# Performance work log

Hardware: AMD Instinct MI355X
Metric: run time of the kernel (lower is better)

## Reference

```python
import jax, jax.numpy as jnp
import numpy as np

MARGIN = 0.0  # init kwarg margin=0


def setup_inputs() -> dict:
    key = jax.random.key(0)
    k1, k2 = jax.random.split(key)
    inputs = jax.random.normal(k1, (4096, 2048), dtype=jnp.float32)
    targets = jax.random.randint(k2, (4096,), 0, 64, dtype=jnp.int64)
    return {"inputs": inputs, "targets": targets}


def _last_true_index(cond):
    # cond: (n, n) bool. Original torch loop zeros leading True entries until one
    # remains -> keeps the LAST True index per row.
    n = cond.shape[1]
    return (n - 1) - jnp.argmax(cond[:, ::-1], axis=1)


def reference(inputs, targets):
    n = inputs.shape[0]
    INF = jnp.asarray(jnp.inf, dtype=inputs.dtype)

    # pairwise euclidean distances: ||xi||^2 + ||xj||^2 - 2 xi.xj, clamp, sqrt
    sq = jnp.sum(inputs * inputs, axis=1)
    dist = sq[:, None] + sq[None, :] - 2.0 * (inputs @ inputs.T)
    dist = jnp.sqrt(jnp.clip(dist, 1e-12))  # (n, n)

    same = targets[:, None] == targets[None, :]  # (n, n) same-label mask

    # hardest positive / hardest negative per row
    dist_ap = jnp.where(same, dist, -INF).max(axis=1)
    dist_an = jnp.where(same, INF, dist).min(axis=1)

    # tie-broken indices (last occurrence, matching the torch loop)
    p = _last_true_index((dist == dist_ap[:, None]) & same)      # hardest pos idx
    q = _last_true_index((dist == dist_an[:, None]) & (~same))   # hardest neg idx

    # an2 = dist(hardest_pos_i, hardest_neg_i)
    dist_an2 = dist[p, q]

    # maskc: labels differing from both anchor's label and hardest-negative's label
    lbl_q = targets[q]
    maskc = (targets[None, :] != targets[:, None]) & (targets[None, :] != lbl_q[:, None])

    dist_q = dist[q]  # (n, n): distance rows of the hardest negatives
    ok_min = jnp.where(maskc, dist_q, INF).min(axis=1)
    r = _last_true_index((dist_q == ok_min[:, None]) & maskc)

    dist_an3 = dist[jnp.arange(n), r]  # dist(anchor, third-class sample)
    dist_an4 = dist_q[jnp.arange(n), r]  # dist(hardest neg, third-class sample) == ok_min

    # MarginRankingLoss(margin, reduce=False) with y=1: relu(ap - an + margin)
    loss = jax.nn.relu(dist_ap - dist_an + MARGIN)
    loss3 = jnp.abs(dist_an - dist_an2)
    loss4 = jnp.abs(dist_an3 - dist_an4)
    return (loss + loss3 + loss4).sum() / n
```

## Files before the change

### kernel.cpp

```cpp
#include <hip/hip_runtime.h>
#include <hip/hip_bf16.h>
#include <cstdint>

#define N_DIM 4096
#define K_DIM 2048
#define NKT 32
#define QSCALE 24.0f
#define QINV (1.0f / 24.0f)

typedef float floatx4 __attribute__((ext_vector_type(4)));
typedef int intx4 __attribute__((ext_vector_type(4)));
typedef unsigned short ushort8 __attribute__((ext_vector_type(8)));
typedef unsigned long long ull;

__device__ __forceinline__ unsigned short f2bf(float f) {
    unsigned int u = __builtin_bit_cast(unsigned int, f);
    unsigned int r = (u + 0x7fffu + ((u >> 16) & 1u)) >> 16;
    return (unsigned short)r;
}

__device__ __forceinline__ float bf2f(unsigned short b) {
    return __uint_as_float(((unsigned)b) << 16);
}

__device__ __forceinline__ void gld_lds16(const void* g, void* l) {
    __builtin_amdgcn_global_load_lds(
        (const __attribute__((address_space(1))) unsigned int*)g,
        (__attribute__((address_space(3))) unsigned int*)l,
        16, 0, 0);
}

__global__ __launch_bounds__(256)
void prep_kernel(const float* __restrict__ X, char* __restrict__ Qt,
                 int* __restrict__ sqi) {
    const int row = blockIdx.x;
    const int tid = threadIdx.x;
    const float* xr = X + (size_t)row * K_DIM;
    floatx4 a = *(const floatx4*)(xr + tid * 8);
    floatx4 b = *(const floatx4*)(xr + tid * 8 + 4);
    int s = 0;
    unsigned lo = 0, hi = 0;
#pragma unroll
    for (int e = 0; e < 4; ++e) {
        int v = __float2int_rn(a[e] * QSCALE);
        v = min(127, max(-127, v));
        s += v * v;
        lo |= ((unsigned)(v & 0xff)) << (8 * e);
        int w = __float2int_rn(b[e] * QSCALE);
        w = min(127, max(-127, w));
        s += w * w;
        hi |= ((unsigned)(w & 0xff)) << (8 * e);
    }
    *(int2*)(Qt + ((size_t)(tid >> 1) * 4096 + row) * 16 + (tid & 1) * 8) =
        make_int2((int)lo, (int)hi);
#pragma unroll
    for (int off = 32; off; off >>= 1) s += __shfl_down(s, off);
    __shared__ int wsum[4];
    const int wave = tid >> 6, lane = tid & 63;
    if (lane == 0) wsum[wave] = s;
    __syncthreads();
    if (tid == 0) sqi[row] = wsum[0] + wsum[1] + wsum[2] + wsum[3];
}

#define BAR() __builtin_amdgcn_s_barrier()
#define PRIO1() __builtin_amdgcn_s_setprio(1)
#define PRIO0() __builtin_amdgcn_s_setprio(0)
#define VMCNT4() asm volatile("s_waitcnt vmcnt(4)" ::: "memory")
#define VMCNT0() asm volatile("s_waitcnt vmcnt(0)" ::: "memory")
#define MM8(MHI, AF) { _Pragma("unroll") for (int n_ = 0; n_ < 4; ++n_) { \
    _Pragma("unroll") for (int m_ = 0; m_ < 4; ++m_) { \
        acc[MHI][n_][m_] = __builtin_amdgcn_mfma_i32_16x16x64_i8( \
            AF[m_], bfv[n_], acc[MHI][n_][m_], 0, 0, 0); } } }
#define KTB 262144
#define STG_B(KT, BB) { \
    gld_lds16(bSt + (size_t)(KT) * KTB,        lds + (BB) + 16384 + widB); \
    gld_lds16(bSt + (size_t)(KT) * KTB + 2048, lds + (BB) + 24576 + widB); }
#define STG_A(KT, BB) { \
    gld_lds16(aSt + (size_t)(KT) * KTB,        lds + (BB) + widB); \
    gld_lds16(aSt + (size_t)(KT) * KTB + 2048, lds + (BB) + 8192 + widB); }

__global__ __launch_bounds__(512, 2)
void gemm_dist(const char* __restrict__ Qt, const int* __restrict__ sqi,
               unsigned short* __restrict__ Db) {
    __shared__ char lds[98304];
    const int tid = threadIdx.x;
    const int wid = tid >> 6, lane = tid & 63;
    const int wr = wid >> 2, wc = wid & 3;
    const int fr = lane & 15, ksub = lane >> 4;
    const int widB = wid * 1024;

    int rA[4], rB[4];
#pragma unroll
    for (int m = 0; m < 4; ++m) rA[m] = (ksub * 128 + m * 16 + fr) * 16;
#pragma unroll
    for (int n = 0; n < 4; ++n) rB[n] = (ksub * 128 + (wc & 1) * 64 + n * 16 + fr) * 16;
    const int aRegOff = wr * 8192;
    const int bRegOff = 16384 + (wc >> 1) * 8192;

    const int swz = (blockIdx.x & 7) * 32 + (blockIdx.x >> 3);
    const int bi = swz >> 4, bj = swz & 15;
    const int rowC0 = bi * 256, colC0 = bj * 256;

    const int srow = tid & 127;
    const int sks = tid >> 7;
    const char* aSt = Qt + ((size_t)sks * 4096 + rowC0 + srow) * 16;
    const char* bSt = Qt + ((size_t)sks * 4096 + colC0 + srow) * 16;

    intx4 acc[2][4][4];
#pragma unroll
    for (int a0 = 0; a0 < 2; ++a0)
#pragma unroll
    for (int a1 = 0; a1 < 4; ++a1)
#pragma unroll
    for (int a2 = 0; a2 < 4; ++a2) acc[a0][a1][a2] = (intx4){0, 0, 0, 0};
    intx4 aflo[4], afhi[4], bfv[4];

    STG_B(0, 0); STG_A(0, 0);
    STG_B(1, 32768); STG_A(1, 32768);
    VMCNT4();
    BAR();

    int cb = 0, sb = 65536;
    for (int t = 0; t < NKT; ++t) {
        const bool pf = (t < NKT - 2);
        const char* bufA = lds + cb + aRegOff;
        const char* bufBp = lds + cb + bRegOff;
#pragma unroll
        for (int m = 0; m < 4; ++m) aflo[m] = *(const intx4*)(bufA + rA[m]);
#pragma unroll
        for (int n = 0; n < 4; ++n) bfv[n] = *(const intx4*)(bufBp + rB[n]);
        if (pf) STG_B(t + 2, sb);
        BAR(); PRIO1(); MM8(0, aflo); PRIO0();
#pragma unroll
        for (int m = 0; m < 4; ++m) afhi[m] = *(const intx4*)(bufA + 1024 + rA[m]);
        if (pf) { STG_A(t + 2, sb); VMCNT4(); } else { VMCNT0(); }
        BAR(); PRIO1(); MM8(1, afhi); PRIO0();
        cb += 32768; if (cb >= 98304) cb = 0;
        sb += 32768; if (sb >= 98304) sb = 0;
    }

#pragma unroll
    for (int MH = 0; MH < 2; ++MH)
#pragma unroll
    for (int n = 0; n < 4; ++n) {
        const int col = colC0 + wc * 64 + n * 16 + fr;
        const int sqc = sqi[col];
#pragma unroll
        for (int m = 0; m < 4; ++m) {
            const int row0 = rowC0 + wr * 128 + MH * 64 + m * 16 + ksub * 4;
#pragma unroll
            for (int r = 0; r < 4; ++r) {
                const int v = sqi[row0 + r] + sqc - 2 * acc[MH][n][m][r];
                const float d = (v > 0) ? sqrtf((float)v) * QINV : 1e-6f;
                Db[(size_t)(row0 + r) * N_DIM + col] = f2bf(d);
            }
        }
    }
}

__global__ __launch_bounds__(256)
void stats_loss(const unsigned short* __restrict__ Db, const int* __restrict__ tgt,
                float* __restrict__ lossArr) {
    const int i = blockIdx.x, tid = threadIdx.x;
    const int ti = tgt[i];
    const unsigned short* row = Db + (size_t)i * N_DIM;
    ull kmax = 0ULL, kmin = ~0ULL;
#pragma unroll
    for (int it = 0; it < 2; ++it) {
        const int j0 = (it * 256 + tid) * 8;
        ushort8 d = *(const ushort8*)(row + j0);
        intx4 ta = *(const intx4*)(tgt + j0);
        intx4 tb = *(const intx4*)(tgt + j0 + 4);
#pragma unroll
        for (int e = 0; e < 8; ++e) {
            const int j = j0 + e;
            const int tl = (e < 4) ? ta[e] : tb[e - 4];
            const ull db = (ull)d[e] << 32;
            if (tl == ti) { ull k = db | (unsigned)j;  if (k > kmax) kmax = k; }
            else          { ull k = db | (unsigned)~j; if (k < kmin) kmin = k; }
        }
    }
    __shared__ ull sM[256], sN[256];
    sM[tid] = kmax; sN[tid] = kmin;
    __syncthreads();
    for (int off = 128; off; off >>= 1) {
        if (tid < off) {
            if (sM[tid + off] > sM[tid]) sM[tid] = sM[tid + off];
            if (sN[tid + off] < sN[tid]) sN[tid] = sN[tid + off];
        }
        __syncthreads();
    }
    const ull km = sM[0], kn = sN[0];
    const float ap = bf2f((unsigned short)(km >> 32));
    const int p = (int)(unsigned)(km & 0xFFFFFFFFu);
    const float an = bf2f((unsigned short)(kn >> 32));
    const int q = (int)~(unsigned)(kn & 0xFFFFFFFFu);
    __syncthreads();

    const int lq = tgt[q];
    const unsigned short* rowq = Db + (size_t)q * N_DIM;
    ull kr = ~0ULL;
#pragma unroll
    for (int it = 0; it < 2; ++it) {
        const int j0 = (it * 256 + tid) * 8;
        ushort8 d = *(const ushort8*)(rowq + j0);
        intx4 ta = *(const intx4*)(tgt + j0);
        intx4 tb = *(const intx4*)(tgt + j0 + 4);
#pragma unroll
        for (int e = 0; e < 8; ++e) {
            const int j = j0 + e;
            const int tl = (e < 4) ? ta[e] : tb[e - 4];
            if (tl != ti && tl != lq) {
                ull k = ((ull)d[e] << 32) | (unsigned)~j;
                if (k < kr) kr = k;
            }
        }
    }
    sN[tid] = kr;
    __syncthreads();
    for (int off = 128; off; off >>= 1) {
        if (tid < off) { if (sN[tid + off] < sN[tid]) sN[tid] = sN[tid + off]; }
        __syncthreads();
    }
    if (tid == 0) {
        const ull kk = sN[0];
        const float okmin = bf2f((unsigned short)(kk >> 32));
        const int r = (int)~(unsigned)(kk & 0xFFFFFFFFu);
        const float an2 = bf2f(Db[(size_t)p * N_DIM + q]);
        const float an3 = bf2f(Db[(size_t)i * N_DIM + r]);
        lossArr[i] = fmaxf(ap - an, 0.f) + fabsf(an - an2) + fabsf(an3 - okmin);
    }
}

__global__ __launch_bounds__(256)
void finred(const float* __restrict__ lossArr, float* __restrict__ out) {
    const int tid = threadIdx.x;
    float s = 0.f;
    for (int j = tid; j < N_DIM; j += 256) s += lossArr[j];
#pragma unroll
    for (int off = 32; off; off >>= 1) s += __shfl_down(s, off);
    __shared__ float w[4];
    const int wave = tid >> 6, lane = tid & 63;
    if (lane == 0) w[wave] = s;
    __syncthreads();
    if (tid == 0) out[0] = (w[0] + w[1] + w[2] + w[3]) * (1.0f / (float)N_DIM);
}

extern "C" void kernel_launch(void* const* d_in, const int* in_sizes, int n_in,
                              void* d_out, int out_size, void* d_ws, size_t ws_size,
                              hipStream_t stream) {
    const float* X = (const float*)d_in[0];
    const int* tgt = (const int*)d_in[1];
    float* out = (float*)d_out;

    char* w = (char*)d_ws;
    char* Qt = w;
    unsigned short* Db = (unsigned short*)(w + ((size_t)16 << 20));
    int* sqi = (int*)(w + ((size_t)80 << 20));
    float* lossArr = (float*)(sqi + N_DIM);

    prep_kernel<<<N_DIM, 256, 0, stream>>>(X, Qt, sqi);
    gemm_dist<<<256, 512, 0, stream>>>(Qt, sqi, Db);
    stats_loss<<<N_DIM, 256, 0, stream>>>(Db, tgt, lossArr);
    finred<<<1, 256, 0, stream>>>(lossArr, out);
}
```

Measured before the change: 76.82 us.

## Use 1024-thread GEMM blocks with 16 waves and single-phase K loop

The int8 distance GEMM now runs 1024 threads (16 waves in a 4x4 grid) per 256x256 tile instead of 512 threads, each holding one 64x64 accumulator set instead of two. The split A/B staging with two barriers per K step becomes one combined stage with a single barrier, and the wait count changes to match. This aims for more latency hiding and fewer barriers per step, at the cost of lower per-wave register reuse and one block per CU with 96KB LDS.

New measurement: 77.08 us. No clear change (+0.3%).

```diff
diff --git a/kernel.cpp b/kernel.cpp
--- a/kernel.cpp
+++ b/kernel.cpp
@@ -65,21 +65,14 @@
 #define BAR() __builtin_amdgcn_s_barrier()
 #define PRIO1() __builtin_amdgcn_s_setprio(1)
 #define PRIO0() __builtin_amdgcn_s_setprio(0)
-#define VMCNT4() asm volatile("s_waitcnt vmcnt(4)" ::: "memory")
+#define VMCNT2() asm volatile("s_waitcnt vmcnt(2)" ::: "memory")
 #define VMCNT0() asm volatile("s_waitcnt vmcnt(0)" ::: "memory")
-#define MM8(MHI, AF) { _Pragma("unroll") for (int n_ = 0; n_ < 4; ++n_) { \
-    _Pragma("unroll") for (int m_ = 0; m_ < 4; ++m_) { \
-        acc[MHI][n_][m_] = __builtin_amdgcn_mfma_i32_16x16x64_i8( \
-            AF[m_], bfv[n_], acc[MHI][n_][m_], 0, 0, 0); } } }
 #define KTB 262144
-#define STG_B(KT, BB) { \
-    gld_lds16(bSt + (size_t)(KT) * KTB,        lds + (BB) + 16384 + widB); \
-    gld_lds16(bSt + (size_t)(KT) * KTB + 2048, lds + (BB) + 24576 + widB); }
-#define STG_A(KT, BB) { \
-    gld_lds16(aSt + (size_t)(KT) * KTB,        lds + (BB) + widB); \
-    gld_lds16(aSt + (size_t)(KT) * KTB + 2048, lds + (BB) + 8192 + widB); }
-
-__global__ __launch_bounds__(512, 2)
+#define STG(KT, BB) { \
+    gld_lds16(aSt + (size_t)(KT) * KTB, lds + (BB) + widB); \
+    gld_lds16(bSt + (size_t)(KT) * KTB, lds + (BB) + 16384 + widB); }
+
+__global__ __launch_bounds__(1024)
 void gemm_dist(const char* __restrict__ Qt, const int* __restrict__ sqi,
                unsigned short* __restrict__ Db) {
     __shared__ char lds[98304];
@@ -91,66 +84,62 @@
 
     int rA[4], rB[4];
 #pragma unroll
-    for (int m = 0; m < 4; ++m) rA[m] = (ksub * 128 + m * 16 + fr) * 16;
-#pragma unroll
-    for (int n = 0; n < 4; ++n) rB[n] = (ksub * 128 + (wc & 1) * 64 + n * 16 + fr) * 16;
-    const int aRegOff = wr * 8192;
-    const int bRegOff = 16384 + (wc >> 1) * 8192;
+    for (int m = 0; m < 4; ++m) rA[m] = (ksub * 256 + wr * 64 + m * 16 + fr) * 16;
+#pragma unroll
+    for (int n = 0; n < 4; ++n) rB[n] = 16384 + (ksub * 256 + wc * 64 + n * 16 + fr) * 16;
 
     const int swz = (blockIdx.x & 7) * 32 + (blockIdx.x >> 3);
     const int bi = swz >> 4, bj = swz & 15;
     const int rowC0 = bi * 256, colC0 = bj * 256;
 
-    const int srow = tid & 127;
-    const int sks = tid >> 7;
+    const int srow = tid & 255;
+    const int sks = tid >> 8;
     const char* aSt = Qt + ((size_t)sks * 4096 + rowC0 + srow) * 16;
     const char* bSt = Qt + ((size_t)sks * 4096 + colC0 + srow) * 16;
 
-    intx4 acc[2][4][4];
-#pragma unroll
-    for (int a0 = 0; a0 < 2; ++a0)
+    intx4 acc[4][4];
 #pragma unroll
     for (int a1 = 0; a1 < 4; ++a1)
 #pragma unroll
-    for (int a2 = 0; a2 < 4; ++a2) acc[a0][a1][a2] = (intx4){0, 0, 0, 0};
-    intx4 aflo[4], afhi[4], bfv[4];
-
-    STG_B(0, 0); STG_A(0, 0);
-    STG_B(1, 32768); STG_A(1, 32768);
-    VMCNT4();
+    for (int a2 = 0; a2 < 4; ++a2) acc[a1][a2] = (intx4){0, 0, 0, 0};
+    intx4 af[4], bfv[4];
+
+    STG(0, 0);
+    STG(1, 32768);
+    VMCNT2();
     BAR();
 
     int cb = 0, sb = 65536;
     for (int t = 0; t < NKT; ++t) {
-        const bool pf = (t < NKT - 2);
-        const char* bufA = lds + cb + aRegOff;
-        const char* bufBp = lds + cb + bRegOff;
-#pragma unroll
-        for (int m = 0; m < 4; ++m) aflo[m] = *(const intx4*)(bufA + rA[m]);
-#pragma unroll
-        for (int n = 0; n < 4; ++n) bfv[n] = *(const intx4*)(bufBp + rB[n]);
-        if (pf) STG_B(t + 2, sb);
-        BAR(); PRIO1(); MM8(0, aflo); PRIO0();
-#pragma unroll
-        for (int m = 0; m < 4; ++m) afhi[m] = *(const intx4*)(bufA + 1024 + rA[m]);
-        if (pf) { STG_A(t + 2, sb); VMCNT4(); } else { VMCNT0(); }
-        BAR(); PRIO1(); MM8(1, afhi); PRIO0();
+        if (t < NKT - 2) STG(t + 2, sb);
+#pragma unroll
+        for (int m = 0; m < 4; ++m) af[m] = *(const intx4*)(lds + cb + rA[m]);
+#pragma unroll
+        for (int n = 0; n < 4; ++n) bfv[n] = *(const intx4*)(lds + cb + rB[n]);
+        PRIO1();
+#pragma unroll
+        for (int n = 0; n < 4; ++n)
+#pragma unroll
+        for (int m = 0; m < 4; ++m)
+            acc[n][m] = __builtin_amdgcn_mfma_i32_16x16x64_i8(
+                af[m], bfv[n], acc[n][m], 0, 0, 0);
+        PRIO0();
+        if (t < NKT - 2) { VMCNT2(); } else if (t == NKT - 2) { VMCNT0(); }
+        BAR();
         cb += 32768; if (cb >= 98304) cb = 0;
         sb += 32768; if (sb >= 98304) sb = 0;
     }
 
-#pragma unroll
-    for (int MH = 0; MH < 2; ++MH)
 #pragma unroll
     for (int n = 0; n < 4; ++n) {
         const int col = colC0 + wc * 64 + n * 16 + fr;
         const int sqc = sqi[col];
 #pragma unroll
         for (int m = 0; m < 4; ++m) {
-            const int row0 = rowC0 + wr * 128 + MH * 64 + m * 16 + ksub * 4;
+            const int row0 = rowC0 + wr * 64 + m * 16 + ksub * 4;
 #pragma unroll
             for (int r = 0; r < 4; ++r) {
-                const int v = sqi[row0 + r] + sqc - 2 * acc[MH][n][m][r];
+                const int v = sqi[row0 + r] + sqc - 2 * acc[n][m][r];
                 const float d = (v > 0) ? sqrtf((float)v) * QINV : 1e-6f;
                 Db[(size_t)(row0 + r) * N_DIM + col] = f2bf(d);
             }
@@ -260,7 +249,7 @@
     float* lossArr = (float*)(sqi + N_DIM);
 
     prep_kernel<<<N_DIM, 256, 0, stream>>>(X, Qt, sqi);
-    gemm_dist<<<256, 512, 0, stream>>>(Qt, sqi, Db);
+    gemm_dist<<<256, 1024, 0, stream>>>(Qt, sqi, Db);
     stats_loss<<<N_DIM, 256, 0, stream>>>(Db, tgt, lossArr);
     finred<<<1, 256, 0, stream>>>(lossArr, out);
 }
```
